# Performance work log

Measured on AMD Instinct MI355X. Metric: run time of the kernel, lower is better.

## Reference

```python
import jax, jax.numpy as jnp
import numpy as np

SCALE = 8
MAX_DEPTH = 81.0
PI = 3.1415926535


def setup_inputs() -> dict:
    key = jax.random.key(0)
    ks = jax.random.split(key, 13)
    B, C, H8, W8 = 16, 128, 44, 144
    d = {"x": jax.random.normal(ks[0], (B, C, H8, W8), jnp.float32)}
    chans = [128, 64, 32, 16, 8, 4]  # reduction chain of 1x1 convs
    for i in range(5):
        d[f"w{i}"] = jax.random.normal(ks[1 + 2 * i], (chans[i + 1], chans[i]), jnp.float32) * 0.05
        d[f"b{i}"] = jnp.zeros((chans[i + 1],), jnp.float32)
    d["wc"] = jax.random.normal(ks[11], (3, 4), jnp.float32) * 0.05  # final 4->3 1x1 conv
    d["bc"] = jnp.zeros((3,), jnp.float32)
    return d


def _conv1x1(x, w, b):
    # x: [B,C,H,W], w: [O,C] -> [B,O,H,W]
    return jnp.einsum('bchw,oc->bohw', x, w) + b[None, :, None, None]


def reference(x, w0, b0, w1, b1, w2, b2, w3, b3, w4, b4, wc, bc):
    elu = jax.nn.elu
    h = elu(_conv1x1(x, w0, b0))
    h = elu(_conv1x1(h, w1, b1))
    h = elu(_conv1x1(h, w2, b2))
    h = elu(_conv1x1(h, w3, b3))
    h = _conv1x1(h, w4, b4)          # [B,4,H8,W8], no activation on last reduction
    y = _conv1x1(h, wc, bc)          # [B,3,H8,W8]

    theta = jax.nn.sigmoid(y[:, 0]) * PI / 6.0
    phi = jax.nn.sigmoid(y[:, 1]) * PI * 2.0
    dist = jax.nn.sigmoid(y[:, 2]) * MAX_DEPTH

    st = jnp.sin(theta)
    n = jnp.stack([st * jnp.cos(phi), st * jnp.sin(phi), jnp.cos(theta)], axis=1)  # [B,3,H8,W8]
    # F.normalize(p=2, dim=1, eps=1e-12)
    norm = jnp.maximum(jnp.sqrt(jnp.sum(n * n, axis=1, keepdims=True)), 1e-12)
    n = n / norm
    plane = jnp.concatenate([n, dist[:, None]], axis=1)  # [B,4,H8,W8]

    # repeat_interleave upsample by SCALE on H then W
    pe = jnp.repeat(jnp.repeat(plane, SCALE, axis=2), SCALE, axis=3)  # [B,4,H,W]
    B, _, H, W = pe.shape

    # local-plane coordinate grids (tiled arange pattern per torch.Tensor.repeat)
    u = (jnp.tile(jnp.arange(SCALE, dtype=jnp.float32), W // SCALE) - (SCALE - 1) * 0.5) / SCALE  # [W]
    v = (jnp.tile(jnp.arange(SCALE, dtype=jnp.float32), H // SCALE) - (SCALE - 1) * 0.5) / SCALE  # [H]

    depth = pe[:, 3] / (pe[:, 0] * u[None, None, :] + pe[:, 1] * v[None, :, None] + pe[:, 2])
    return depth[:, None]  # [B,1,H,W]
```

## Files before the change

### kernel.cpp

```cpp
#include <hip/hip_runtime.h>
#include <hip/hip_bf16.h>

#define NB   16
#define C0   128
#define HH   44
#define WW   144
#define HW   (HH * WW)
#define NPOS (NB * HW)
#define SC   8
#define WOUT (WW * SC)
#define HOUT (HH * SC)
#define PI_F 3.1415926535f

typedef __attribute__((ext_vector_type(8))) short bf8;
typedef __attribute__((ext_vector_type(4))) float f4;
typedef unsigned short ushort_t;

#define F0 0
#define F1 8192
#define F2 10240
#define NWT 10752

__device__ __forceinline__ unsigned short f2bf(float f) {
    union { float f; unsigned u; } v; v.f = f;
    unsigned r = v.u + 0x7FFFu + ((v.u >> 16) & 1u);
    return (unsigned short)(r >> 16);
}
__device__ __forceinline__ float eluf(float x) {
    return x > 0.f ? x : (__expf(x) - 1.f);
}
__device__ __forceinline__ float sigmoidf(float x) {
    return 1.f / (1.f + __expf(-x));
}

__global__ void prep_w(const float* __restrict__ w0, const float* __restrict__ w1,
                       const float* __restrict__ w2, ushort_t* __restrict__ ws) {
    int i = blockIdx.x * 256 + (int)threadIdx.x;
    if (i < 8192) {
        int j = i & 7, lane = (i >> 3) & 63, ch = i >> 9;
        int q = lane >> 4, n = lane & 15, kk = ch & 3, t = ch >> 2;
        ws[F0 + i] = f2bf(w0[(t * 16 + n) * 128 + kk * 32 + q * 8 + j]);
    } else if (i < 10240) {
        int i2 = i - 8192;
        int j = i2 & 7, lane = (i2 >> 3) & 63, ch = i2 >> 9;
        int q = lane >> 4, n = lane & 15, kk = ch & 1, t = ch >> 1;
        ws[F1 + i2] = f2bf(w1[(t * 16 + n) * 64 + kk * 32 + q * 8 + j]);
    } else if (i < NWT) {
        int i2 = i - 10240;
        int j = i2 & 7, lane = (i2 >> 3) & 63;
        int q = lane >> 4, n = lane & 15;
        ws[F2 + i2] = f2bf(w2[n * 32 + q * 8 + j]);
    }
}

#define H1B 0
#define H2B 1152
#define H3F 1792

__global__ __launch_bounds__(256, 4)
void lpg_mfma(const float* __restrict__ x, const ushort_t* __restrict__ wsb,
              const float* __restrict__ b0, const float* __restrict__ b1,
              const float* __restrict__ b2, const float* __restrict__ b3,
              const float* __restrict__ w3, const float* __restrict__ w4,
              const float* __restrict__ b4,
              const float* __restrict__ wc, const float* __restrict__ bc,
              float* __restrict__ out) {
    __shared__ __align__(16) ushort_t hbuf[4][2432];

    const int tid  = (int)threadIdx.x;
    const int lane = tid & 63;
    const int wid  = tid >> 6;
    const int q    = lane >> 4;
    const int n    = lane & 15;

    const int pm = blockIdx.x * 64 + wid * 16 + n;
    const int bm = pm / HW;
    const int hwm = pm - bm * HW;

    const float* xb = x + (size_t)bm * (C0 * HW) + hwm;
    float xr[32];
#pragma unroll
    for (int kk = 0; kk < 4; ++kk)
#pragma unroll
        for (int j = 0; j < 8; ++j)
            xr[kk * 8 + j] = xb[(kk * 32 + q * 8 + j) * HW];

    bf8 A[4];
#pragma unroll
    for (int kk = 0; kk < 4; ++kk) {
        bf8 a;
#pragma unroll
        for (int j = 0; j < 8; j += 2) {
            __hip_bfloat162 p = __float22bfloat162_rn(
                make_float2(xr[kk * 8 + j], xr[kk * 8 + j + 1]));
            union { __hip_bfloat162 b; short s[2]; } u; u.b = p;
            a[j] = u.s[0]; a[j + 1] = u.s[1];
        }
        A[kk] = a;
    }

    f4 acc[4];
#pragma unroll
    for (int t = 0; t < 4; ++t) {
        const float bb = b0[t * 16 + n];
        acc[t] = (f4){bb, bb, bb, bb};
    }
#pragma unroll
    for (int t = 0; t < 4; ++t) {
        bf8 B[4];
#pragma unroll
        for (int kk = 0; kk < 4; ++kk)
            B[kk] = *(const bf8*)(wsb + F0 + (t * 4 + kk) * 512 + lane * 8);
#pragma unroll
        for (int kk = 0; kk < 4; ++kk)
            acc[t] = __builtin_amdgcn_mfma_f32_16x16x32_bf16(A[kk], B[kk], acc[t], 0, 0, 0);
    }

    ushort_t* hb = &hbuf[wid][0];
#pragma unroll
    for (int t = 0; t < 4; ++t)
#pragma unroll
        for (int r = 0; r < 4; ++r)
            hb[H1B + (q * 4 + r) * 72 + t * 16 + n] = f2bf(eluf(acc[t][r]));

    bf8 A1[2];
#pragma unroll
    for (int kk = 0; kk < 2; ++kk)
        A1[kk] = *(const bf8*)(hb + H1B + n * 72 + kk * 32 + q * 8);
    f4 acc1[2];
#pragma unroll
    for (int t = 0; t < 2; ++t) {
        const float bb = b1[t * 16 + n];
        acc1[t] = (f4){bb, bb, bb, bb};
    }
#pragma unroll
    for (int t = 0; t < 2; ++t)
#pragma unroll
        for (int kk = 0; kk < 2; ++kk) {
            bf8 B = *(const bf8*)(wsb + F1 + (t * 2 + kk) * 512 + lane * 8);
            acc1[t] = __builtin_amdgcn_mfma_f32_16x16x32_bf16(A1[kk], B, acc1[t], 0, 0, 0);
        }
#pragma unroll
    for (int t = 0; t < 2; ++t)
#pragma unroll
        for (int r = 0; r < 4; ++r)
            hb[H2B + (q * 4 + r) * 40 + t * 16 + n] = f2bf(eluf(acc1[t][r]));

    bf8 A2 = *(const bf8*)(hb + H2B + n * 40 + q * 8);
    bf8 B2 = *(const bf8*)(wsb + F2 + lane * 8);
    const float bb2 = b2[n];
    f4 acc2 = (f4){bb2, bb2, bb2, bb2};
    acc2 = __builtin_amdgcn_mfma_f32_16x16x32_bf16(A2, B2, acc2, 0, 0, 0);
    float* h3f = (float*)(hb + H3F);
#pragma unroll
    for (int r = 0; r < 4; ++r)
        h3f[(q * 4 + r) * 20 + n] = eluf(acc2[r]);

    float h3[16];
#pragma unroll
    for (int i = 0; i < 4; ++i) {
        f4 v = *(const f4*)(h3f + n * 20 + i * 4);
        h3[4 * i + 0] = v[0]; h3[4 * i + 1] = v[1];
        h3[4 * i + 2] = v[2]; h3[4 * i + 3] = v[3];
    }

    float h4v[8];
#pragma unroll
    for (int o = 0; o < 8; ++o) {
        float a = b3[o];
#pragma unroll
        for (int c = 0; c < 16; ++c) a = fmaf(h3[c], w3[o * 16 + c], a);
        h4v[o] = eluf(a);
    }
    float h5v[4];
#pragma unroll
    for (int o = 0; o < 4; ++o) {
        float a = b4[o];
#pragma unroll
        for (int c = 0; c < 8; ++c) a = fmaf(h4v[c], w4[o * 8 + c], a);
        h5v[o] = a;
    }
    float y0 = bc[0], y1 = bc[1], y2 = bc[2];
#pragma unroll
    for (int c = 0; c < 4; ++c) {
        y0 = fmaf(h5v[c], wc[0 * 4 + c], y0);
        y1 = fmaf(h5v[c], wc[1 * 4 + c], y1);
        y2 = fmaf(h5v[c], wc[2 * 4 + c], y2);
    }

    const float theta = sigmoidf(y0) * (PI_F / 6.0f);
    const float phi   = sigmoidf(y1) * (PI_F * 2.0f);
    const float dist  = sigmoidf(y2) * 81.0f;
    const float st = __sinf(theta), ct = __cosf(theta);
    const float sp = __sinf(phi),   cp = __cosf(phi);
    float nx = st * cp, ny = st * sp, nz = ct;
    const float inv = rsqrtf(fmaxf(nx * nx + ny * ny + nz * nz, 1e-24f));
    nx *= inv; ny *= inv; nz *= inv;

    const int hh = hwm / WW;
    const int wp = hwm - hh * WW;
    float* op = out + ((size_t)bm * HOUT + (size_t)hh * SC) * WOUT + (size_t)wp * SC;

    float nxu[8];
#pragma unroll
    for (int j = 0; j < 8; ++j) nxu[j] = nx * ((j - 3.5f) * 0.125f);

#pragma unroll
    for (int ii = 0; ii < 2; ++ii) {
        const int i = q * 2 + ii;
        const float den0 = fmaf(ny, (i - 3.5f) * 0.125f, nz);
        float d[8];
#pragma unroll
        for (int j = 0; j < 8; ++j)
            d[j] = dist * __builtin_amdgcn_rcpf(den0 + nxu[j]);
        float* row = op + (size_t)i * WOUT;
        *reinterpret_cast<float4*>(row)     = make_float4(d[0], d[1], d[2], d[3]);
        *reinterpret_cast<float4*>(row + 4) = make_float4(d[4], d[5], d[6], d[7]);
    }
}

extern "C" void kernel_launch(void* const* d_in, const int* in_sizes, int n_in,
                              void* d_out, int out_size, void* d_ws, size_t ws_size,
                              hipStream_t stream) {
    const float* x  = (const float*)d_in[0];
    const float* w0 = (const float*)d_in[1];  const float* b0 = (const float*)d_in[2];
    const float* w1 = (const float*)d_in[3];  const float* b1 = (const float*)d_in[4];
    const float* w2 = (const float*)d_in[5];  const float* b2 = (const float*)d_in[6];
    const float* w3 = (const float*)d_in[7];  const float* b3 = (const float*)d_in[8];
    const float* w4 = (const float*)d_in[9];  const float* b4 = (const float*)d_in[10];
    const float* wc = (const float*)d_in[11]; const float* bc = (const float*)d_in[12];
    ushort_t* ws = (ushort_t*)d_ws;
    float* out = (float*)d_out;

    hipLaunchKernelGGL(prep_w, dim3((NWT + 255) / 256), dim3(256), 0, stream,
                       w0, w1, w2, ws);
    hipLaunchKernelGGL(lpg_mfma, dim3(NPOS / 64), dim3(256), 0, stream,
                       x, ws, b0, b1, b2, b3, w3, w4, b4, wc, bc, out);
}
```

Baseline: 122.6 us.

## Split fused MFMA kernel into conv0 kernel plus per-thread scalar tail kernel

Splits the single fused kernel in two. The first kernel runs only the 128->64 MFMA conv and writes the bf16 activations to global workspace in channel-major layout. The second kernel assigns one pixel per thread, does the 64->32 and 32->16 convs with scalar FMAs in fp32 using transposed weights, runs the tail, and writes all 8x8 output rows. This removes the LDS round trips and the redundant tail work that was repeated across quad lanes, at the cost of a global round trip for a roughly 2.9M-element bf16 intermediate, an extra launch, and heavy per-thread register use.

```diff
diff --git a/kernel.cpp b/kernel.cpp
--- a/kernel.cpp
+++ b/kernel.cpp
@@ -16,15 +16,19 @@
 typedef __attribute__((ext_vector_type(4))) float f4;
 typedef unsigned short ushort_t;
 
-#define F0 0
-#define F1 8192
-#define F2 10240
-#define NWT 10752
-
-__device__ __forceinline__ unsigned short f2bf(float f) {
+#define WS_F0   0
+#define WS_WT1  16384
+#define WS_WT2  24576
+#define WS_H1   32768
+#define NPREP   10752
+
+__device__ __forceinline__ unsigned f2bf(float f) {
     union { float f; unsigned u; } v; v.f = f;
     unsigned r = v.u + 0x7FFFu + ((v.u >> 16) & 1u);
-    return (unsigned short)(r >> 16);
+    return r >> 16;
+}
+__device__ __forceinline__ float bf2f(ushort_t s) {
+    union { unsigned u; float f; } v; v.u = ((unsigned)s) << 16; return v.f;
 }
 __device__ __forceinline__ float eluf(float x) {
     return x > 0.f ? x : (__expf(x) - 1.f);
@@ -34,47 +38,36 @@
 }
 
 __global__ void prep_w(const float* __restrict__ w0, const float* __restrict__ w1,
-                       const float* __restrict__ w2, ushort_t* __restrict__ ws) {
+                       const float* __restrict__ w2, ushort_t* __restrict__ f0,
+                       float* __restrict__ wt1, float* __restrict__ wt2) {
     int i = blockIdx.x * 256 + (int)threadIdx.x;
     if (i < 8192) {
         int j = i & 7, lane = (i >> 3) & 63, ch = i >> 9;
         int q = lane >> 4, n = lane & 15, kk = ch & 3, t = ch >> 2;
-        ws[F0 + i] = f2bf(w0[(t * 16 + n) * 128 + kk * 32 + q * 8 + j]);
+        f0[i] = (ushort_t)f2bf(w0[(t * 16 + n) * 128 + kk * 32 + q * 8 + j]);
     } else if (i < 10240) {
         int i2 = i - 8192;
-        int j = i2 & 7, lane = (i2 >> 3) & 63, ch = i2 >> 9;
-        int q = lane >> 4, n = lane & 15, kk = ch & 1, t = ch >> 1;
-        ws[F1 + i2] = f2bf(w1[(t * 16 + n) * 64 + kk * 32 + q * 8 + j]);
-    } else if (i < NWT) {
+        int c = i2 >> 5, o = i2 & 31;
+        wt1[c * 32 + o] = w1[o * 64 + c];
+    } else if (i < NPREP) {
         int i2 = i - 10240;
-        int j = i2 & 7, lane = (i2 >> 3) & 63;
-        int q = lane >> 4, n = lane & 15;
-        ws[F2 + i2] = f2bf(w2[n * 32 + q * 8 + j]);
-    }
-}
-
-#define H1B 0
-#define H2B 1152
-#define H3F 1792
+        int c = i2 >> 4, o = i2 & 15;
+        wt2[c * 16 + o] = w2[o * 32 + c];
+    }
+}
 
 __global__ __launch_bounds__(256, 4)
-void lpg_mfma(const float* __restrict__ x, const ushort_t* __restrict__ wsb,
-              const float* __restrict__ b0, const float* __restrict__ b1,
-              const float* __restrict__ b2, const float* __restrict__ b3,
-              const float* __restrict__ w3, const float* __restrict__ w4,
-              const float* __restrict__ b4,
-              const float* __restrict__ wc, const float* __restrict__ bc,
-              float* __restrict__ out) {
-    __shared__ __align__(16) ushort_t hbuf[4][2432];
-
+void k1_conv0(const float* __restrict__ x, const ushort_t* __restrict__ fr,
+              const float* __restrict__ b0, ushort_t* __restrict__ h1) {
     const int tid  = (int)threadIdx.x;
     const int lane = tid & 63;
     const int wid  = tid >> 6;
     const int q    = lane >> 4;
     const int n    = lane & 15;
 
-    const int pm = blockIdx.x * 64 + wid * 16 + n;
-    const int bm = pm / HW;
+    const int p0w = blockIdx.x * 64 + wid * 16;
+    const int pm  = p0w + n;
+    const int bm  = pm / HW;
     const int hwm = pm - bm * HW;
 
     const float* xb = x + (size_t)bm * (C0 * HW) + hwm;
@@ -91,9 +84,9 @@
         bf8 a;
 #pragma unroll
         for (int j = 0; j < 8; j += 2) {
-            __hip_bfloat162 p = __float22bfloat162_rn(
+            __hip_bfloat162 pck = __float22bfloat162_rn(
                 make_float2(xr[kk * 8 + j], xr[kk * 8 + j + 1]));
-            union { __hip_bfloat162 b; short s[2]; } u; u.b = p;
+            union { __hip_bfloat162 b; short s[2]; } u; u.b = pck;
             a[j] = u.s[0]; a[j + 1] = u.s[1];
         }
         A[kk] = a;
@@ -110,82 +103,83 @@
         bf8 B[4];
 #pragma unroll
         for (int kk = 0; kk < 4; ++kk)
-            B[kk] = *(const bf8*)(wsb + F0 + (t * 4 + kk) * 512 + lane * 8);
+            B[kk] = *(const bf8*)(fr + (t * 4 + kk) * 512 + lane * 8);
 #pragma unroll
         for (int kk = 0; kk < 4; ++kk)
             acc[t] = __builtin_amdgcn_mfma_f32_16x16x32_bf16(A[kk], B[kk], acc[t], 0, 0, 0);
     }
 
-    ushort_t* hb = &hbuf[wid][0];
-#pragma unroll
-    for (int t = 0; t < 4; ++t)
-#pragma unroll
-        for (int r = 0; r < 4; ++r)
-            hb[H1B + (q * 4 + r) * 72 + t * 16 + n] = f2bf(eluf(acc[t][r]));
-
-    bf8 A1[2];
-#pragma unroll
-    for (int kk = 0; kk < 2; ++kk)
-        A1[kk] = *(const bf8*)(hb + H1B + n * 72 + kk * 32 + q * 8);
-    f4 acc1[2];
-#pragma unroll
-    for (int t = 0; t < 2; ++t) {
-        const float bb = b1[t * 16 + n];
-        acc1[t] = (f4){bb, bb, bb, bb};
-    }
-#pragma unroll
-    for (int t = 0; t < 2; ++t)
-#pragma unroll
-        for (int kk = 0; kk < 2; ++kk) {
-            bf8 B = *(const bf8*)(wsb + F1 + (t * 2 + kk) * 512 + lane * 8);
-            acc1[t] = __builtin_amdgcn_mfma_f32_16x16x32_bf16(A1[kk], B, acc1[t], 0, 0, 0);
-        }
-#pragma unroll
-    for (int t = 0; t < 2; ++t)
-#pragma unroll
-        for (int r = 0; r < 4; ++r)
-            hb[H2B + (q * 4 + r) * 40 + t * 16 + n] = f2bf(eluf(acc1[t][r]));
-
-    bf8 A2 = *(const bf8*)(hb + H2B + n * 40 + q * 8);
-    bf8 B2 = *(const bf8*)(wsb + F2 + lane * 8);
-    const float bb2 = b2[n];
-    f4 acc2 = (f4){bb2, bb2, bb2, bb2};
-    acc2 = __builtin_amdgcn_mfma_f32_16x16x32_bf16(A2, B2, acc2, 0, 0, 0);
-    float* h3f = (float*)(hb + H3F);
-#pragma unroll
-    for (int r = 0; r < 4; ++r)
-        h3f[(q * 4 + r) * 20 + n] = eluf(acc2[r]);
+#pragma unroll
+    for (int t = 0; t < 4; ++t) {
+        unsigned lo = f2bf(eluf(acc[t][0])) | (f2bf(eluf(acc[t][1])) << 16);
+        unsigned hi = f2bf(eluf(acc[t][2])) | (f2bf(eluf(acc[t][3])) << 16);
+        uint2 v; v.x = lo; v.y = hi;
+        *reinterpret_cast<uint2*>(h1 + (size_t)(t * 16 + n) * NPOS + p0w + 4 * q) = v;
+    }
+}
+
+__global__ __launch_bounds__(256, 1)
+void k2_rest(const ushort_t* __restrict__ h1,
+             const float* __restrict__ wt1, const float* __restrict__ b1,
+             const float* __restrict__ wt2, const float* __restrict__ b2,
+             const float* __restrict__ w3,  const float* __restrict__ b3,
+             const float* __restrict__ w4,  const float* __restrict__ b4,
+             const float* __restrict__ wc,  const float* __restrict__ bc,
+             float* __restrict__ out) {
+    const int p  = blockIdx.x * 256 + (int)threadIdx.x;
+    const int b  = p / HW;
+    const int hw = p - b * HW;
+
+    float h2[32];
+#pragma unroll
+    for (int o = 0; o < 32; ++o) h2[o] = b1[o];
+#pragma unroll
+    for (int c = 0; c < 64; ++c) {
+        const float hv = bf2f(h1[(size_t)c * NPOS + p]);
+        const float* wt = wt1 + c * 32;
+#pragma unroll
+        for (int o = 0; o < 32; ++o) h2[o] = fmaf(hv, wt[o], h2[o]);
+    }
+#pragma unroll
+    for (int o = 0; o < 32; ++o) h2[o] = eluf(h2[o]);
 
     float h3[16];
 #pragma unroll
-    for (int i = 0; i < 4; ++i) {
-        f4 v = *(const f4*)(h3f + n * 20 + i * 4);
-        h3[4 * i + 0] = v[0]; h3[4 * i + 1] = v[1];
-        h3[4 * i + 2] = v[2]; h3[4 * i + 3] = v[3];
-    }
-
-    float h4v[8];
+    for (int o = 0; o < 16; ++o) h3[o] = b2[o];
+#pragma unroll
+    for (int c = 0; c < 32; ++c) {
+        const float hv = h2[c];
+        const float* wt = wt2 + c * 16;
+#pragma unroll
+        for (int o = 0; o < 16; ++o) h3[o] = fmaf(hv, wt[o], h3[o]);
+    }
+#pragma unroll
+    for (int o = 0; o < 16; ++o) h3[o] = eluf(h3[o]);
+
+    float h4[8];
 #pragma unroll
     for (int o = 0; o < 8; ++o) {
         float a = b3[o];
 #pragma unroll
         for (int c = 0; c < 16; ++c) a = fmaf(h3[c], w3[o * 16 + c], a);
-        h4v[o] = eluf(a);
-    }
-    float h5v[4];
+        h4[o] = eluf(a);
+    }
+
+    float h5[4];
 #pragma unroll
     for (int o = 0; o < 4; ++o) {
         float a = b4[o];
 #pragma unroll
-        for (int c = 0; c < 8; ++c) a = fmaf(h4v[c], w4[o * 8 + c], a);
-        h5v[o] = a;
-    }
+        for (int c = 0; c < 8; ++c) a = fmaf(h4[c], w4[o * 8 + c], a);
+        h5[o] = a;
+    }
+
     float y0 = bc[0], y1 = bc[1], y2 = bc[2];
 #pragma unroll
     for (int c = 0; c < 4; ++c) {
-        y0 = fmaf(h5v[c], wc[0 * 4 + c], y0);
-        y1 = fmaf(h5v[c], wc[1 * 4 + c], y1);
-        y2 = fmaf(h5v[c], wc[2 * 4 + c], y2);
+        y0 = fmaf(h5[c], wc[0 * 4 + c], y0);
+        y1 = fmaf(h5[c], wc[1 * 4 + c], y1);
+        y2 = fmaf(h5[c], wc[2 * 4 + c], y2);
     }
 
     const float theta = sigmoidf(y0) * (PI_F / 6.0f);
@@ -197,17 +191,16 @@
     const float inv = rsqrtf(fmaxf(nx * nx + ny * ny + nz * nz, 1e-24f));
     nx *= inv; ny *= inv; nz *= inv;
 
-    const int hh = hwm / WW;
-    const int wp = hwm - hh * WW;
-    float* op = out + ((size_t)bm * HOUT + (size_t)hh * SC) * WOUT + (size_t)wp * SC;
+    const int h = hw / WW;
+    const int w = hw - h * WW;
+    float* op = out + ((size_t)b * HOUT + (size_t)h * SC) * WOUT + (size_t)w * SC;
 
     float nxu[8];
 #pragma unroll
     for (int j = 0; j < 8; ++j) nxu[j] = nx * ((j - 3.5f) * 0.125f);
 
 #pragma unroll
-    for (int ii = 0; ii < 2; ++ii) {
-        const int i = q * 2 + ii;
+    for (int i = 0; i < 8; ++i) {
         const float den0 = fmaf(ny, (i - 3.5f) * 0.125f, nz);
         float d[8];
 #pragma unroll
@@ -229,11 +222,18 @@
     const float* w3 = (const float*)d_in[7];  const float* b3 = (const float*)d_in[8];
     const float* w4 = (const float*)d_in[9];  const float* b4 = (const float*)d_in[10];
     const float* wc = (const float*)d_in[11]; const float* bc = (const float*)d_in[12];
-    ushort_t* ws = (ushort_t*)d_ws;
     float* out = (float*)d_out;
 
-    hipLaunchKernelGGL(prep_w, dim3((NWT + 255) / 256), dim3(256), 0, stream,
-                       w0, w1, w2, ws);
-    hipLaunchKernelGGL(lpg_mfma, dim3(NPOS / 64), dim3(256), 0, stream,
-                       x, ws, b0, b1, b2, b3, w3, w4, b4, wc, bc, out);
-}
+    char* ws = (char*)d_ws;
+    ushort_t* f0  = (ushort_t*)(ws + WS_F0);
+    float*    wt1 = (float*)(ws + WS_WT1);
+    float*    wt2 = (float*)(ws + WS_WT2);
+    ushort_t* h1  = (ushort_t*)(ws + WS_H1);
+
+    hipLaunchKernelGGL(prep_w, dim3((NPREP + 255) / 256), dim3(256), 0, stream,
+                       w0, w1, w2, f0, wt1, wt2);
+    hipLaunchKernelGGL(k1_conv0, dim3(NPOS / 64), dim3(256), 0, stream,
+                       x, f0, b0, h1);
+    hipLaunchKernelGGL(k2_rest, dim3(NPOS / 256), dim3(256), 0, stream,
+                       h1, wt1, b1, wt2, b2, w3, b3, w4, b4, wc, bc, out);
+}
```

After: 148.7 us. +21.3%, slower.

## Switch conv chain to 32x32x16 MFMA with 32 positions per wave

Applied to the files above, without the earlier changes.

Restructures the fused 1x1-conv chain to use 32x32x16 bf16 MFMA tiles, so each wave handles 32 pixel positions instead of 16. Weight pre-packing is redone for the new fragment layout, and the third layer is zero-padded to 32 outputs. Each block now covers 128 positions, which halves the grid and raises per-thread register and LDS use (launch bounds drop to 3 waves per SIMD). Output stores become nontemporal to avoid polluting cache with the large write-only upsampled tensor.

```diff
diff --git a/kernel.cpp b/kernel.cpp
--- a/kernel.cpp
+++ b/kernel.cpp
@@ -12,154 +12,163 @@
 #define HOUT (HH * SC)
 #define PI_F 3.1415926535f
 
-typedef __attribute__((ext_vector_type(8))) short bf8;
-typedef __attribute__((ext_vector_type(4))) float f4;
+typedef __attribute__((ext_vector_type(8)))  short bf8;
+typedef __attribute__((ext_vector_type(4)))  float f4;
+typedef __attribute__((ext_vector_type(16))) float f16v;
 typedef unsigned short ushort_t;
 
 #define F0 0
 #define F1 8192
 #define F2 10240
-#define NWT 10752
-
-__device__ __forceinline__ unsigned short f2bf(float f) {
+#define NWT 11264
+
+__device__ __forceinline__ unsigned f2bf(float f) {
     union { float f; unsigned u; } v; v.f = f;
     unsigned r = v.u + 0x7FFFu + ((v.u >> 16) & 1u);
-    return (unsigned short)(r >> 16);
+    return r >> 16;
 }
 __device__ __forceinline__ float eluf(float x) {
     return x > 0.f ? x : (__expf(x) - 1.f);
 }
 __device__ __forceinline__ float sigmoidf(float x) {
     return 1.f / (1.f + __expf(-x));
+}
+__device__ __forceinline__ int crow(int r, int g) {
+    return (r & 3) + 8 * (r >> 2) + 4 * g;
 }
 
 __global__ void prep_w(const float* __restrict__ w0, const float* __restrict__ w1,
                        const float* __restrict__ w2, ushort_t* __restrict__ ws) {
     int i = blockIdx.x * 256 + (int)threadIdx.x;
+    int j = i & 7, lane = (i >> 3) & 63;
+    int n = lane & 31, g = lane >> 5;
     if (i < 8192) {
-        int j = i & 7, lane = (i >> 3) & 63, ch = i >> 9;
-        int q = lane >> 4, n = lane & 15, kk = ch & 3, t = ch >> 2;
-        ws[F0 + i] = f2bf(w0[(t * 16 + n) * 128 + kk * 32 + q * 8 + j]);
+        int c = i >> 9;
+        int s = c & 7, t = c >> 3;
+        ws[F0 + i] = (ushort_t)f2bf(w0[(t * 32 + n) * 128 + s * 16 + g * 8 + j]);
     } else if (i < 10240) {
         int i2 = i - 8192;
-        int j = i2 & 7, lane = (i2 >> 3) & 63, ch = i2 >> 9;
-        int q = lane >> 4, n = lane & 15, kk = ch & 1, t = ch >> 1;
-        ws[F1 + i2] = f2bf(w1[(t * 16 + n) * 64 + kk * 32 + q * 8 + j]);
+        int s = i2 >> 9;
+        ws[F1 + i2] = (ushort_t)f2bf(w1[n * 64 + s * 16 + g * 8 + j]);
     } else if (i < NWT) {
         int i2 = i - 10240;
-        int j = i2 & 7, lane = (i2 >> 3) & 63;
-        int q = lane >> 4, n = lane & 15;
-        ws[F2 + i2] = f2bf(w2[n * 32 + q * 8 + j]);
-    }
-}
-
-#define H1B 0
-#define H2B 1152
-#define H3F 1792
-
-__global__ __launch_bounds__(256, 4)
-void lpg_mfma(const float* __restrict__ x, const ushort_t* __restrict__ wsb,
-              const float* __restrict__ b0, const float* __restrict__ b1,
-              const float* __restrict__ b2, const float* __restrict__ b3,
-              const float* __restrict__ w3, const float* __restrict__ w4,
-              const float* __restrict__ b4,
-              const float* __restrict__ wc, const float* __restrict__ bc,
-              float* __restrict__ out) {
-    __shared__ __align__(16) ushort_t hbuf[4][2432];
+        int s = i2 >> 9;
+        ws[F2 + i2] = (n < 16) ? (ushort_t)f2bf(w2[n * 32 + s * 16 + g * 8 + j])
+                               : (ushort_t)0;
+    }
+}
+
+__global__ __launch_bounds__(256, 3)
+void lpg32(const float* __restrict__ x, const ushort_t* __restrict__ wsb,
+           const float* __restrict__ b0, const float* __restrict__ b1,
+           const float* __restrict__ b2, const float* __restrict__ b3,
+           const float* __restrict__ w3, const float* __restrict__ w4,
+           const float* __restrict__ b4,
+           const float* __restrict__ wc, const float* __restrict__ bc,
+           float* __restrict__ out) {
+    __shared__ __align__(16) ushort_t hb1s[4][2304];
+    __shared__ __align__(16) ushort_t hb2s[4][1280];
+    __shared__ __align__(16) float    hb3s[4][640];
 
     const int tid  = (int)threadIdx.x;
     const int lane = tid & 63;
     const int wid  = tid >> 6;
-    const int q    = lane >> 4;
-    const int n    = lane & 15;
-
-    const int pm = blockIdx.x * 64 + wid * 16 + n;
-    const int bm = pm / HW;
+    const int m    = lane & 31;
+    const int g    = lane >> 5;
+
+    const int pm  = blockIdx.x * 128 + wid * 32 + m;
+    const int bm  = pm / HW;
     const int hwm = pm - bm * HW;
-
     const float* xb = x + (size_t)bm * (C0 * HW) + hwm;
-    float xr[32];
-#pragma unroll
-    for (int kk = 0; kk < 4; ++kk)
+
+    bf8 A[8];
+#pragma unroll
+    for (int s = 0; s < 8; ++s) {
+        float xr[8];
 #pragma unroll
         for (int j = 0; j < 8; ++j)
-            xr[kk * 8 + j] = xb[(kk * 32 + q * 8 + j) * HW];
-
-    bf8 A[4];
-#pragma unroll
-    for (int kk = 0; kk < 4; ++kk) {
+            xr[j] = xb[(s * 16 + g * 8 + j) * HW];
         bf8 a;
 #pragma unroll
         for (int j = 0; j < 8; j += 2) {
-            __hip_bfloat162 p = __float22bfloat162_rn(
-                make_float2(xr[kk * 8 + j], xr[kk * 8 + j + 1]));
-            union { __hip_bfloat162 b; short s[2]; } u; u.b = p;
-            a[j] = u.s[0]; a[j + 1] = u.s[1];
+            __hip_bfloat162 pck = __float22bfloat162_rn(make_float2(xr[j], xr[j + 1]));
+            union { __hip_bfloat162 b; short s2[2]; } u; u.b = pck;
+            a[j] = u.s2[0]; a[j + 1] = u.s2[1];
         }
-        A[kk] = a;
-    }
-
-    f4 acc[4];
-#pragma unroll
-    for (int t = 0; t < 4; ++t) {
-        const float bb = b0[t * 16 + n];
-        acc[t] = (f4){bb, bb, bb, bb};
-    }
-#pragma unroll
-    for (int t = 0; t < 4; ++t) {
-        bf8 B[4];
-#pragma unroll
-        for (int kk = 0; kk < 4; ++kk)
-            B[kk] = *(const bf8*)(wsb + F0 + (t * 4 + kk) * 512 + lane * 8);
-#pragma unroll
-        for (int kk = 0; kk < 4; ++kk)
-            acc[t] = __builtin_amdgcn_mfma_f32_16x16x32_bf16(A[kk], B[kk], acc[t], 0, 0, 0);
-    }
-
-    ushort_t* hb = &hbuf[wid][0];
-#pragma unroll
-    for (int t = 0; t < 4; ++t)
-#pragma unroll
-        for (int r = 0; r < 4; ++r)
-            hb[H1B + (q * 4 + r) * 72 + t * 16 + n] = f2bf(eluf(acc[t][r]));
-
-    bf8 A1[2];
-#pragma unroll
-    for (int kk = 0; kk < 2; ++kk)
-        A1[kk] = *(const bf8*)(hb + H1B + n * 72 + kk * 32 + q * 8);
-    f4 acc1[2];
-#pragma unroll
-    for (int t = 0; t < 2; ++t) {
-        const float bb = b1[t * 16 + n];
-        acc1[t] = (f4){bb, bb, bb, bb};
-    }
-#pragma unroll
-    for (int t = 0; t < 2; ++t)
-#pragma unroll
-        for (int kk = 0; kk < 2; ++kk) {
-            bf8 B = *(const bf8*)(wsb + F1 + (t * 2 + kk) * 512 + lane * 8);
-            acc1[t] = __builtin_amdgcn_mfma_f32_16x16x32_bf16(A1[kk], B, acc1[t], 0, 0, 0);
-        }
-#pragma unroll
-    for (int t = 0; t < 2; ++t)
-#pragma unroll
-        for (int r = 0; r < 4; ++r)
-            hb[H2B + (q * 4 + r) * 40 + t * 16 + n] = f2bf(eluf(acc1[t][r]));
-
-    bf8 A2 = *(const bf8*)(hb + H2B + n * 40 + q * 8);
-    bf8 B2 = *(const bf8*)(wsb + F2 + lane * 8);
-    const float bb2 = b2[n];
-    f4 acc2 = (f4){bb2, bb2, bb2, bb2};
-    acc2 = __builtin_amdgcn_mfma_f32_16x16x32_bf16(A2, B2, acc2, 0, 0, 0);
-    float* h3f = (float*)(hb + H3F);
-#pragma unroll
-    for (int r = 0; r < 4; ++r)
-        h3f[(q * 4 + r) * 20 + n] = eluf(acc2[r]);
+        A[s] = a;
+    }
+
+    f16v acc0, acc1;
+    {
+        const float bb0 = b0[m], bb1 = b0[32 + m];
+#pragma unroll
+        for (int r = 0; r < 16; ++r) { acc0[r] = bb0; acc1[r] = bb1; }
+    }
+#pragma unroll
+    for (int s = 0; s < 8; ++s) {
+        bf8 B = *(const bf8*)(wsb + F0 + (0 * 8 + s) * 512 + lane * 8);
+        acc0 = __builtin_amdgcn_mfma_f32_32x32x16_bf16(A[s], B, acc0, 0, 0, 0);
+    }
+#pragma unroll
+    for (int s = 0; s < 8; ++s) {
+        bf8 B = *(const bf8*)(wsb + F0 + (1 * 8 + s) * 512 + lane * 8);
+        acc1 = __builtin_amdgcn_mfma_f32_32x32x16_bf16(A[s], B, acc1, 0, 0, 0);
+    }
+
+    ushort_t* h1p = &hb1s[wid][0];
+#pragma unroll
+    for (int r = 0; r < 16; ++r) {
+        const int row = crow(r, g);
+        h1p[row * 72 + m]      = (ushort_t)f2bf(eluf(acc0[r]));
+        h1p[row * 72 + 32 + m] = (ushort_t)f2bf(eluf(acc1[r]));
+    }
+
+    bf8 A1[4];
+#pragma unroll
+    for (int s = 0; s < 4; ++s)
+        A1[s] = *(const bf8*)(h1p + m * 72 + s * 16 + g * 8);
+    f16v c1;
+    {
+        const float bb = b1[m];
+#pragma unroll
+        for (int r = 0; r < 16; ++r) c1[r] = bb;
+    }
+#pragma unroll
+    for (int s = 0; s < 4; ++s) {
+        bf8 B = *(const bf8*)(wsb + F1 + s * 512 + lane * 8);
+        c1 = __builtin_amdgcn_mfma_f32_32x32x16_bf16(A1[s], B, c1, 0, 0, 0);
+    }
+    ushort_t* h2p = &hb2s[wid][0];
+#pragma unroll
+    for (int r = 0; r < 16; ++r)
+        h2p[crow(r, g) * 40 + m] = (ushort_t)f2bf(eluf(c1[r]));
+
+    bf8 A2[2];
+#pragma unroll
+    for (int s = 0; s < 2; ++s)
+        A2[s] = *(const bf8*)(h2p + m * 40 + s * 16 + g * 8);
+    f16v c2;
+    {
+        const float bb = (m < 16) ? b2[m & 15] : 0.f;
+#pragma unroll
+        for (int r = 0; r < 16; ++r) c2[r] = bb;
+    }
+#pragma unroll
+    for (int s = 0; s < 2; ++s) {
+        bf8 B = *(const bf8*)(wsb + F2 + s * 512 + lane * 8);
+        c2 = __builtin_amdgcn_mfma_f32_32x32x16_bf16(A2[s], B, c2, 0, 0, 0);
+    }
+    float* h3p = &hb3s[wid][0];
+    if (m < 16) {
+#pragma unroll
+        for (int r = 0; r < 16; ++r)
+            h3p[crow(r, g) * 20 + m] = eluf(c2[r]);
+    }
 
     float h3[16];
 #pragma unroll
     for (int i = 0; i < 4; ++i) {
-        f4 v = *(const f4*)(h3f + n * 20 + i * 4);
+        f4 v = *(const f4*)(h3p + m * 20 + i * 4);
         h3[4 * i + 0] = v[0]; h3[4 * i + 1] = v[1];
         h3[4 * i + 2] = v[2]; h3[4 * i + 3] = v[3];
     }
@@ -206,16 +215,18 @@
     for (int j = 0; j < 8; ++j) nxu[j] = nx * ((j - 3.5f) * 0.125f);
 
 #pragma unroll
-    for (int ii = 0; ii < 2; ++ii) {
-        const int i = q * 2 + ii;
+    for (int ii = 0; ii < 4; ++ii) {
+        const int i = g * 4 + ii;
         const float den0 = fmaf(ny, (i - 3.5f) * 0.125f, nz);
         float d[8];
 #pragma unroll
         for (int j = 0; j < 8; ++j)
             d[j] = dist * __builtin_amdgcn_rcpf(den0 + nxu[j]);
         float* row = op + (size_t)i * WOUT;
-        *reinterpret_cast<float4*>(row)     = make_float4(d[0], d[1], d[2], d[3]);
-        *reinterpret_cast<float4*>(row + 4) = make_float4(d[4], d[5], d[6], d[7]);
+        f4 v0 = (f4){d[0], d[1], d[2], d[3]};
+        f4 v1 = (f4){d[4], d[5], d[6], d[7]};
+        __builtin_nontemporal_store(v0, reinterpret_cast<f4*>(row));
+        __builtin_nontemporal_store(v1, reinterpret_cast<f4*>(row + 4));
     }
 }
 
@@ -234,6 +245,6 @@
 
     hipLaunchKernelGGL(prep_w, dim3((NWT + 255) / 256), dim3(256), 0, stream,
                        w0, w1, w2, ws);
-    hipLaunchKernelGGL(lpg_mfma, dim3(NPOS / 64), dim3(256), 0, stream,
+    hipLaunchKernelGGL(lpg32, dim3(NPOS / 128), dim3(256), 0, stream,
                        x, ws, b0, b1, b2, b3, w3, w4, b4, wc, bc, out);
 }
```

Result: no change. 122.9 us (+0.3%).
